# Performance work log

Measured on AMD Instinct MI355X. Metric: run time of the kernel, lower is better.

The kernel has to match this reference:

```python
import jax, jax.numpy as jnp
import numpy as np

N_NODES = 100000
N_EDGES = 800000
IN_CH = 128
HID = 128
OUT_CH = 64


def setup_inputs() -> dict:
    key = jax.random.key(0)
    ks = jax.random.split(key, 8)
    x = jax.random.normal(ks[0], (N_NODES, IN_CH), dtype=jnp.float32)
    edge_index = jax.random.randint(ks[1], (2, N_EDGES), 0, N_NODES, dtype=jnp.int64)
    # GCNConv weights (Glorot) and zero biases
    def glorot(k, fan_in, fan_out):
        s = jnp.sqrt(6.0 / (fan_in + fan_out))
        return jax.random.uniform(k, (fan_in, fan_out), jnp.float32, -s, s)
    return {
        "x": x,
        "edge_index": edge_index,
        "W1": glorot(ks[2], IN_CH, HID), "b1": jnp.zeros((HID,), jnp.float32),
        "W2": glorot(ks[3], HID, HID),   "b2": jnp.zeros((HID,), jnp.float32),
        "W3": glorot(ks[4], HID, OUT_CH), "b3": jnp.zeros((OUT_CH,), jnp.float32),
    }


def _gcn_conv(h, W, b, src, dst, norm, self_norm, n_nodes):
    """PyG GCNConv: out = D^-1/2 (A+I) D^-1/2 (h W) + b.
    Self-loop contribution added densely (self_norm = dinv^2) to avoid
    appending N extra edges."""
    h = h @ W  # [N, F_out]
    msg = h[src] * norm[:, None]  # [E, F_out] gathered + normalized messages
    agg = jax.ops.segment_sum(msg, dst, num_segments=n_nodes)
    return agg + h * self_norm[:, None] + b


def reference(x, edge_index, W1, b1, W2, b2, W3, b3):
    n_nodes = x.shape[0]
    src = edge_index[0]
    dst = edge_index[1]
    # degrees with self-loops (edge weights = 1)
    deg = jax.ops.segment_sum(jnp.ones_like(src, dtype=x.dtype), dst,
                              num_segments=n_nodes) + 1.0
    dinv = jax.lax.rsqrt(deg)
    norm = dinv[src] * dinv[dst]   # per-edge symmetric normalization
    self_norm = dinv * dinv        # normalization of the i->i self loop

    h = jax.nn.relu(_gcn_conv(x, W1, b1, src, dst, norm, self_norm, n_nodes))
    # dropout is identity in eval mode (training=False)
    h = jax.nn.relu(_gcn_conv(h, W2, b2, src, dst, norm, self_norm, n_nodes))
    out = _gcn_conv(h, W3, b3, src, dst, norm, self_norm, n_nodes)
    return out
```

## Files before the change

kernel.cpp:

```cpp
#include <hip/hip_runtime.h>


#define IN_CH 128

typedef __attribute__((ext_vector_type(8))) short bf16x8;
typedef __attribute__((ext_vector_type(4))) float f32x4;

__device__ inline unsigned short f2bf_rne(float f) {
    unsigned u = __float_as_uint(f);
    unsigned r = (u + 0x7FFFu + ((u >> 16) & 1u)) >> 16;
    return (unsigned short)r;
}
__device__ inline float bf2f(unsigned short h) {
    return __uint_as_float(((unsigned)h) << 16);
}
__device__ inline float bf2f_lo(unsigned m) {
    return __uint_as_float(m << 16);
}
__device__ inline float bf2f_hi(unsigned m) {
    return __uint_as_float(m & 0xffff0000u);
}

__global__ __launch_bounds__(256) void cnt_k(const int* __restrict__ dst,
                                             int* __restrict__ cnt, int E) {
    int e = blockIdx.x * 256 + threadIdx.x;
    if (e < E) atomicAdd(&cnt[dst[e]], 1);
}

__global__ __launch_bounds__(256) void scan1_k(const int* __restrict__ cnt,
                                               int* __restrict__ bsum,
                                               float* __restrict__ dinv, int N) {
    __shared__ int s[256];
    int tid = threadIdx.x;
    int i = blockIdx.x * 256 + tid;
    int v = (i < N) ? cnt[i] : 0;
    if (i < N) dinv[i] = rsqrtf((float)v + 1.0f);
    s[tid] = v;
    __syncthreads();
    for (int off = 128; off > 0; off >>= 1) {
        if (tid < off) s[tid] += s[tid + off];
        __syncthreads();
    }
    if (tid == 0) bsum[blockIdx.x] = s[0];
}

__global__ __launch_bounds__(512) void scan2_k(int* __restrict__ bsum, int nb) {
    __shared__ int s[512];
    __shared__ int carry_s;
    int tid = threadIdx.x;
    if (tid == 0) carry_s = 0;
    __syncthreads();
    for (int base = 0; base < nb; base += 512) {
        int c = carry_s;
        int i = base + tid;
        int v = (i < nb) ? bsum[i] : 0;
        s[tid] = v;
        __syncthreads();
        for (int off = 1; off < 512; off <<= 1) {
            int t = (tid >= off) ? s[tid - off] : 0;
            __syncthreads();
            s[tid] += t;
            __syncthreads();
        }
        if (i < nb) bsum[i] = s[tid] - v + c;
        __syncthreads();
        if (tid == 0) carry_s = c + s[511];
        __syncthreads();
    }
}

__global__ __launch_bounds__(256) void scan3_k(const int* __restrict__ cnt,
                                               const int* __restrict__ bsum,
                                               int* __restrict__ rowptr, int N) {
    __shared__ int s[256];
    int tid = threadIdx.x;
    int i = blockIdx.x * 256 + tid;
    int v = (i < N) ? cnt[i] : 0;
    s[tid] = v;
    __syncthreads();
    for (int off = 1; off < 256; off <<= 1) {
        int t = (tid >= off) ? s[tid - off] : 0;
        __syncthreads();
        s[tid] += t;
        __syncthreads();
    }
    if (i < N) rowptr[i] = s[tid] - v + bsum[blockIdx.x];
}

__device__ inline void convw_one(const float* W, unsigned short* hi, int FOUT, int id) {
    int n = id >> 7, k = id & 127;
    hi[id] = f2bf_rne(W[k * FOUT + n]);
}

__global__ __launch_bounds__(256) void fill_conv_k(
    const int* __restrict__ src, const int* __restrict__ dst,
    const float* __restrict__ dinv, int* __restrict__ rowptr,
    int2* __restrict__ pairs, int E, int fillBlocks,
    const float* __restrict__ W1, const float* __restrict__ W2,
    const float* __restrict__ W3,
    unsigned short* __restrict__ W1h, unsigned short* __restrict__ W2h,
    unsigned short* __restrict__ W3h) {
    if ((int)blockIdx.x < fillBlocks) {
        int e = blockIdx.x * 256 + threadIdx.x;
        if (e < E) {
            int s = src[e], d = dst[e];
            float nrm = dinv[s] * dinv[d];
            int pos = atomicAdd(&rowptr[d], 1);
            pairs[pos] = make_int2(s, __float_as_int(nrm));
        }
    } else {
        int id = (blockIdx.x - fillBlocks) * 256 + threadIdx.x;
        if (id < 16384) convw_one(W1, W1h, 128, id);
        else if (id < 32768) convw_one(W2, W2h, 128, id - 16384);
        else if (id < 40960) convw_one(W3, W3h, 64, id - 32768);
    }
}

__device__ inline bf16x8 cvt8(const float* __restrict__ p) {
    float4 v0 = *(const float4*)p;
    float4 v1 = *(const float4*)(p + 4);
    bf16x8 h;
    h[0] = (short)f2bf_rne(v0.x); h[1] = (short)f2bf_rne(v0.y);
    h[2] = (short)f2bf_rne(v0.z); h[3] = (short)f2bf_rne(v0.w);
    h[4] = (short)f2bf_rne(v1.x); h[5] = (short)f2bf_rne(v1.y);
    h[6] = (short)f2bf_rne(v1.z); h[7] = (short)f2bf_rne(v1.w);
    return h;
}

template <int FOUT, bool AF32>
__global__ __launch_bounds__(256) void mfma_gemm(const float* __restrict__ Af,
                                                 const unsigned short* __restrict__ Ahi,
                                                 const unsigned short* __restrict__ Bhi,
                                                 unsigned short* __restrict__ Thi,
                                                 int N) {
    constexpr int NCT = FOUT / 16;
    constexpr int BSTRIDE = 136;
    constexpr int CSTRIDE = FOUT + 8;
    constexpr int BU = FOUT * BSTRIDE;
    constexpr int CU = 64 * CSTRIDE;
    constexpr int SMEMU = (BU > CU) ? BU : CU;
    __shared__ unsigned short smem[SMEMU];

    const int tid = threadIdx.x;
    const int wv = tid >> 6, lane = tid & 63;
    const int quad = lane >> 4, l16 = lane & 15;
    const int row0 = blockIdx.x * 64 + wv * 16;

#pragma unroll
    for (int it = 0; it < FOUT / 16; ++it) {
        int i = it * 256 + tid;
        int r = i >> 4, c = (i & 15) * 8;
        *(bf16x8*)(&smem[r * BSTRIDE + c]) = *(const bf16x8*)(Bhi + (size_t)r * 128 + c);
    }
    __syncthreads();

    f32x4 acc[NCT];
#pragma unroll
    for (int ct = 0; ct < NCT; ++ct)
        acc[ct] = (f32x4){0.f, 0.f, 0.f, 0.f};

    const int ra = AF32 ? min(row0 + l16, N - 1) : (row0 + l16);

#pragma unroll
    for (int ks = 0; ks < 4; ++ks) {
        const int ko = ks * 32 + quad * 8;
        bf16x8 ah;
        if (AF32) {
            ah = cvt8(Af + (size_t)ra * 128 + ko);
        } else {
            ah = *(const bf16x8*)(Ahi + (size_t)ra * 128 + ko);
        }
#pragma unroll
        for (int ct = 0; ct < NCT; ++ct) {
            bf16x8 bh = *(const bf16x8*)(&smem[(ct * 16 + l16) * BSTRIDE + ko]);
            acc[ct] = __builtin_amdgcn_mfma_f32_16x16x32_bf16(ah, bh, acc[ct], 0, 0, 0);
        }
    }

    __syncthreads();
    const int lrow = wv * 16 + quad * 4;
#pragma unroll
    for (int ct = 0; ct < NCT; ++ct) {
        const int col = ct * 16 + l16;
#pragma unroll
        for (int r = 0; r < 4; ++r)
            smem[(lrow + r) * CSTRIDE + col] = f2bf_rne(acc[ct][r]);
    }
    __syncthreads();
    constexpr int CH = FOUT / 8;
#pragma unroll
    for (int i = 0; i < 64 * CH / 256; ++i) {
        int ci = i * 256 + tid;
        int r = ci / CH, c = (ci % CH) * 8;
        int grow = blockIdx.x * 64 + r;
        if (grow < N)
            *(uint4*)(Thi + (size_t)grow * FOUT + c) = *(const uint4*)&smem[r * CSTRIDE + c];
    }
}

template <int FOUT, bool SPLIT>
__global__ __launch_bounds__(256) void gather_k(const int* __restrict__ rowend,
                                                const int2* __restrict__ pairs,
                                                const float* __restrict__ dinv,
                                                const unsigned short* __restrict__ Thi,
                                                const float* __restrict__ bias,
                                                float* __restrict__ out,
                                                unsigned short* __restrict__ outHi,
                                                int N) {
    const int wave = threadIdx.x >> 6;
    const int lane = threadIdx.x & 63;
    const int row = blockIdx.x * 4 + wave;
    if (row >= N) return;

    const int start = (row == 0) ? 0 : rowend[row - 1];
    const int end = rowend[row];
    const float dr = dinv[row];

    if (FOUT == 128) {
        const unsigned* thi32 = (const unsigned*)Thi;
        unsigned sh = thi32[(size_t)row * 64 + lane];
        float2 bb = *(const float2*)(bias + lane * 2);
        float ax = bb.x + bf2f_lo(sh) * dr * dr;
        float ay = bb.y + bf2f_hi(sh) * dr * dr;

        int j = start;
        if ((j & 1) && j < end) {
            int2 pv = pairs[j];
            unsigned m = thi32[(size_t)pv.x * 64 + lane];
            float n = __int_as_float(pv.y);
            ax += n * bf2f_lo(m);
            ay += n * bf2f_hi(m);
            ++j;
        }
        for (; j + 4 <= end; j += 4) {
            int4 p01 = *(const int4*)(pairs + j);
            int4 p23 = *(const int4*)(pairs + j + 2);
            unsigned m0 = thi32[(size_t)p01.x * 64 + lane];
            unsigned m1 = thi32[(size_t)p01.z * 64 + lane];
            unsigned m2 = thi32[(size_t)p23.x * 64 + lane];
            unsigned m3 = thi32[(size_t)p23.z * 64 + lane];
            float n0 = __int_as_float(p01.y), n1 = __int_as_float(p01.w);
            float n2 = __int_as_float(p23.y), n3 = __int_as_float(p23.w);
            ax += n0 * bf2f_lo(m0); ay += n0 * bf2f_hi(m0);
            ax += n1 * bf2f_lo(m1); ay += n1 * bf2f_hi(m1);
            ax += n2 * bf2f_lo(m2); ay += n2 * bf2f_hi(m2);
            ax += n3 * bf2f_lo(m3); ay += n3 * bf2f_hi(m3);
        }
        for (; j < end; ++j) {
            int2 pv = pairs[j];
            unsigned m = thi32[(size_t)pv.x * 64 + lane];
            float n = __int_as_float(pv.y);
            ax += n * bf2f_lo(m);
            ay += n * bf2f_hi(m);
        }

        if (SPLIT) {
            float vx = fmaxf(ax, 0.f), vy = fmaxf(ay, 0.f);
            ushort2 h;
            h.x = f2bf_rne(vx);
            h.y = f2bf_rne(vy);
            *(ushort2*)(outHi + (size_t)row * 128 + lane * 2) = h;
        } else {
            float2 o; o.x = ax; o.y = ay;
            *(float2*)(out + (size_t)row * 128 + lane * 2) = o;
        }
    } else {
        float acc = bias[lane] + bf2f(Thi[(size_t)row * FOUT + lane]) * dr * dr;

        int j = start;
        if ((j & 1) && j < end) {
            int2 pv = pairs[j];
            acc += __int_as_float(pv.y) * bf2f(Thi[(size_t)pv.x * FOUT + lane]);
            ++j;
        }
        for (; j + 4 <= end; j += 4) {
            int4 p01 = *(const int4*)(pairs + j);
            int4 p23 = *(const int4*)(pairs + j + 2);
            float m0 = bf2f(Thi[(size_t)p01.x * FOUT + lane]);
            float m1 = bf2f(Thi[(size_t)p01.z * FOUT + lane]);
            float m2 = bf2f(Thi[(size_t)p23.x * FOUT + lane]);
            float m3 = bf2f(Thi[(size_t)p23.z * FOUT + lane]);
            acc += __int_as_float(p01.y) * m0 + __int_as_float(p01.w) * m1 +
                   __int_as_float(p23.y) * m2 + __int_as_float(p23.w) * m3;
        }
        for (; j < end; ++j) {
            int2 pv = pairs[j];
            acc += __int_as_float(pv.y) * bf2f(Thi[(size_t)pv.x * FOUT + lane]);
        }
        out[(size_t)row * FOUT + lane] = acc;
    }
}

extern "C" void kernel_launch(void* const* d_in, const int* in_sizes, int n_in,
                              void* d_out, int out_size, void* d_ws, size_t ws_size,
                              hipStream_t stream) {
    const float* x  = (const float*)d_in[0];
    const int* eidx = (const int*)d_in[1];
    const float* W1 = (const float*)d_in[2];
    const float* b1 = (const float*)d_in[3];
    const float* W2 = (const float*)d_in[4];
    const float* b2 = (const float*)d_in[5];
    const float* W3 = (const float*)d_in[6];
    const float* b3 = (const float*)d_in[7];
    float* out = (float*)d_out;

    const int N = in_sizes[0] / IN_CH;
    const int E = in_sizes[1] / 2;
    const int* src = eidx;
    const int* dst = eidx + E;
    const int Npad = ((N + 127) / 128) * 128;
    const int nb = (N + 255) / 256;

    auto align = [](size_t v) { return (v + 255) / 256 * 256; };
    char* p = (char*)d_ws;
    int* cnt = (int*)p;            p += align((size_t)N * 4);
    int* rowptr = (int*)p;         p += align((size_t)N * 4);
    int* bsum = (int*)p;           p += align((size_t)nb * 4);
    float* dinv = (float*)p;       p += align((size_t)N * 4);
    int2* pairs = (int2*)p;        p += align((size_t)E * 8);
    unsigned short* Ahi = (unsigned short*)p;  p += align((size_t)Npad * 128 * 2);
    unsigned short* Thi = (unsigned short*)p;  p += align((size_t)Npad * 128 * 2);
    unsigned short* W1h = (unsigned short*)p;  p += align(128 * 128 * 2);
    unsigned short* W2h = (unsigned short*)p;  p += align(128 * 128 * 2);
    unsigned short* W3h = (unsigned short*)p;

    hipMemsetAsync(cnt, 0, (size_t)N * 4, stream);
    cnt_k<<<(E + 255) / 256, 256, 0, stream>>>(dst, cnt, E);
    scan1_k<<<nb, 256, 0, stream>>>(cnt, bsum, dinv, N);
    scan2_k<<<1, 512, 0, stream>>>(bsum, nb);
    scan3_k<<<nb, 256, 0, stream>>>(cnt, bsum, rowptr, N);
    const int fillBlocks = (E + 255) / 256;
    fill_conv_k<<<fillBlocks + 160, 256, 0, stream>>>(src, dst, dinv, rowptr, pairs,
                                                      E, fillBlocks, W1, W2, W3,
                                                      W1h, W2h, W3h);

    const int gemm_blocks = (N + 63) / 64;
    const int gather_blocks = (N + 3) / 4;

    mfma_gemm<128, true><<<gemm_blocks, 256, 0, stream>>>(x, nullptr, W1h, Thi, N);
    gather_k<128, true><<<gather_blocks, 256, 0, stream>>>(rowptr, pairs, dinv, Thi,
                                                           b1, nullptr, Ahi, N);
    mfma_gemm<128, false><<<gemm_blocks, 256, 0, stream>>>(nullptr, Ahi, W2h, Thi, N);
    gather_k<128, true><<<gather_blocks, 256, 0, stream>>>(rowptr, pairs, dinv, Thi,
                                                           b2, nullptr, Ahi, N);
    mfma_gemm<64, false><<<gemm_blocks, 256, 0, stream>>>(nullptr, Ahi, W3h, Thi, N);
    gather_k<64, false><<<gather_blocks, 256, 0, stream>>>(rowptr, pairs, dinv, Thi,
                                                           b3, out, nullptr, N);
}
```

Baseline: 358.9 us.

## Pad CSR rows to multiples of four and prescale source indices to byte offsets

The CSR edge list now pads each destination row to a multiple of four entries. The padding is zero-filled, so it acts as zero-weight edges that gather row 0. The gather kernels drop their alignment-peel and tail loops and run only the unrolled 4-wide loop. Source indices are stored pre-multiplied by the row byte stride, which removes the 64-bit index multiply in the address computation. The cost is a memset of the larger pairs buffer, up to 3N extra padded edges, and a separate cursor array for the atomic fill.

```diff
diff --git a/kernel.cpp b/kernel.cpp
--- a/kernel.cpp
+++ b/kernel.cpp
@@ -33,9 +33,9 @@
     __shared__ int s[256];
     int tid = threadIdx.x;
     int i = blockIdx.x * 256 + tid;
-    int v = (i < N) ? cnt[i] : 0;
-    if (i < N) dinv[i] = rsqrtf((float)v + 1.0f);
-    s[tid] = v;
+    int vr = (i < N) ? cnt[i] : 0;
+    if (i < N) dinv[i] = rsqrtf((float)vr + 1.0f);
+    s[tid] = (i < N) ? ((vr + 3) & ~3) : 0;
     __syncthreads();
     for (int off = 128; off > 0; off >>= 1) {
         if (tid < off) s[tid] += s[tid + off];
@@ -71,11 +71,12 @@
 
 __global__ __launch_bounds__(256) void scan3_k(const int* __restrict__ cnt,
                                                const int* __restrict__ bsum,
-                                               int* __restrict__ rowptr, int N) {
+                                               int* __restrict__ rowstart,
+                                               int* __restrict__ cur, int N) {
     __shared__ int s[256];
     int tid = threadIdx.x;
     int i = blockIdx.x * 256 + tid;
-    int v = (i < N) ? cnt[i] : 0;
+    int v = (i < N) ? ((cnt[i] + 3) & ~3) : 0;
     s[tid] = v;
     __syncthreads();
     for (int off = 1; off < 256; off <<= 1) {
@@ -84,7 +85,12 @@
         s[tid] += t;
         __syncthreads();
     }
-    if (i < N) rowptr[i] = s[tid] - v + bsum[blockIdx.x];
+    if (i < N) {
+        int st = s[tid] - v + bsum[blockIdx.x];
+        rowstart[i] = st;
+        cur[i] = st;
+        if (i == N - 1) rowstart[N] = st + v;
+    }
 }
 
 __device__ inline void convw_one(const float* W, unsigned short* hi, int FOUT, int id) {
@@ -94,7 +100,7 @@
 
 __global__ __launch_bounds__(256) void fill_conv_k(
     const int* __restrict__ src, const int* __restrict__ dst,
-    const float* __restrict__ dinv, int* __restrict__ rowptr,
+    const float* __restrict__ dinv, int* __restrict__ cur,
     int2* __restrict__ pairs, int E, int fillBlocks,
     const float* __restrict__ W1, const float* __restrict__ W2,
     const float* __restrict__ W3,
@@ -105,8 +111,8 @@
         if (e < E) {
             int s = src[e], d = dst[e];
             float nrm = dinv[s] * dinv[d];
-            int pos = atomicAdd(&rowptr[d], 1);
-            pairs[pos] = make_int2(s, __float_as_int(nrm));
+            int pos = atomicAdd(&cur[d], 1);
+            pairs[pos] = make_int2(s * 256, __float_as_int(nrm));
         }
     } else {
         int id = (blockIdx.x - fillBlocks) * 256 + threadIdx.x;
@@ -199,7 +205,7 @@
 }
 
 template <int FOUT, bool SPLIT>
-__global__ __launch_bounds__(256) void gather_k(const int* __restrict__ rowend,
+__global__ __launch_bounds__(256) void gather_k(const int* __restrict__ rowstart,
                                                 const int2* __restrict__ pairs,
                                                 const float* __restrict__ dinv,
                                                 const unsigned short* __restrict__ Thi,
@@ -212,46 +218,31 @@
     const int row = blockIdx.x * 4 + wave;
     if (row >= N) return;
 
-    const int start = (row == 0) ? 0 : rowend[row - 1];
-    const int end = rowend[row];
+    const int start = rowstart[row];
+    const int end = rowstart[row + 1];
     const float dr = dinv[row];
+    const char* tbase = (const char*)Thi;
 
     if (FOUT == 128) {
-        const unsigned* thi32 = (const unsigned*)Thi;
-        unsigned sh = thi32[(size_t)row * 64 + lane];
+        const int laneB = lane * 4;
+        unsigned sh = *(const unsigned*)(tbase + (size_t)row * 256 + laneB);
         float2 bb = *(const float2*)(bias + lane * 2);
         float ax = bb.x + bf2f_lo(sh) * dr * dr;
         float ay = bb.y + bf2f_hi(sh) * dr * dr;
 
-        int j = start;
-        if ((j & 1) && j < end) {
-            int2 pv = pairs[j];
-            unsigned m = thi32[(size_t)pv.x * 64 + lane];
-            float n = __int_as_float(pv.y);
-            ax += n * bf2f_lo(m);
-            ay += n * bf2f_hi(m);
-            ++j;
-        }
-        for (; j + 4 <= end; j += 4) {
+        for (int j = start; j < end; j += 4) {
             int4 p01 = *(const int4*)(pairs + j);
             int4 p23 = *(const int4*)(pairs + j + 2);
-            unsigned m0 = thi32[(size_t)p01.x * 64 + lane];
-            unsigned m1 = thi32[(size_t)p01.z * 64 + lane];
-            unsigned m2 = thi32[(size_t)p23.x * 64 + lane];
-            unsigned m3 = thi32[(size_t)p23.z * 64 + lane];
+            unsigned m0 = *(const unsigned*)(tbase + (unsigned)p01.x + laneB);
+            unsigned m1 = *(const unsigned*)(tbase + (unsigned)p01.z + laneB);
+            unsigned m2 = *(const unsigned*)(tbase + (unsigned)p23.x + laneB);
+            unsigned m3 = *(const unsigned*)(tbase + (unsigned)p23.z + laneB);
             float n0 = __int_as_float(p01.y), n1 = __int_as_float(p01.w);
             float n2 = __int_as_float(p23.y), n3 = __int_as_float(p23.w);
             ax += n0 * bf2f_lo(m0); ay += n0 * bf2f_hi(m0);
             ax += n1 * bf2f_lo(m1); ay += n1 * bf2f_hi(m1);
             ax += n2 * bf2f_lo(m2); ay += n2 * bf2f_hi(m2);
             ax += n3 * bf2f_lo(m3); ay += n3 * bf2f_hi(m3);
-        }
-        for (; j < end; ++j) {
-            int2 pv = pairs[j];
-            unsigned m = thi32[(size_t)pv.x * 64 + lane];
-            float n = __int_as_float(pv.y);
-            ax += n * bf2f_lo(m);
-            ay += n * bf2f_hi(m);
         }
 
         if (SPLIT) {
@@ -265,27 +256,19 @@
             *(float2*)(out + (size_t)row * 128 + lane * 2) = o;
         }
     } else {
-        float acc = bias[lane] + bf2f(Thi[(size_t)row * FOUT + lane]) * dr * dr;
-
-        int j = start;
-        if ((j & 1) && j < end) {
-            int2 pv = pairs[j];
-            acc += __int_as_float(pv.y) * bf2f(Thi[(size_t)pv.x * FOUT + lane]);
-            ++j;
-        }
-        for (; j + 4 <= end; j += 4) {
+        const int laneB = lane * 2;
+        float acc = bias[lane] +
+                    bf2f(*(const unsigned short*)(tbase + (size_t)row * 128 + laneB)) * dr * dr;
+
+        for (int j = start; j < end; j += 4) {
             int4 p01 = *(const int4*)(pairs + j);
             int4 p23 = *(const int4*)(pairs + j + 2);
-            float m0 = bf2f(Thi[(size_t)p01.x * FOUT + lane]);
-            float m1 = bf2f(Thi[(size_t)p01.z * FOUT + lane]);
-            float m2 = bf2f(Thi[(size_t)p23.x * FOUT + lane]);
-            float m3 = bf2f(Thi[(size_t)p23.z * FOUT + lane]);
+            float m0 = bf2f(*(const unsigned short*)(tbase + ((unsigned)p01.x >> 1) + laneB));
+            float m1 = bf2f(*(const unsigned short*)(tbase + ((unsigned)p01.z >> 1) + laneB));
+            float m2 = bf2f(*(const unsigned short*)(tbase + ((unsigned)p23.x >> 1) + laneB));
+            float m3 = bf2f(*(const unsigned short*)(tbase + ((unsigned)p23.z >> 1) + laneB));
             acc += __int_as_float(p01.y) * m0 + __int_as_float(p01.w) * m1 +
                    __int_as_float(p23.y) * m2 + __int_as_float(p23.w) * m3;
-        }
-        for (; j < end; ++j) {
-            int2 pv = pairs[j];
-            acc += __int_as_float(pv.y) * bf2f(Thi[(size_t)pv.x * FOUT + lane]);
         }
         out[(size_t)row * FOUT + lane] = acc;
     }
@@ -310,14 +293,16 @@
     const int* dst = eidx + E;
     const int Npad = ((N + 127) / 128) * 128;
     const int nb = (N + 255) / 256;
+    const int Emax = E + 3 * N;
 
     auto align = [](size_t v) { return (v + 255) / 256 * 256; };
     char* p = (char*)d_ws;
     int* cnt = (int*)p;            p += align((size_t)N * 4);
-    int* rowptr = (int*)p;         p += align((size_t)N * 4);
+    int* rowstart = (int*)p;       p += align((size_t)(N + 1) * 4);
+    int* cur = (int*)p;            p += align((size_t)N * 4);
     int* bsum = (int*)p;           p += align((size_t)nb * 4);
     float* dinv = (float*)p;       p += align((size_t)N * 4);
-    int2* pairs = (int2*)p;        p += align((size_t)E * 8);
+    int2* pairs = (int2*)p;        p += align((size_t)Emax * 8);
     unsigned short* Ahi = (unsigned short*)p;  p += align((size_t)Npad * 128 * 2);
     unsigned short* Thi = (unsigned short*)p;  p += align((size_t)Npad * 128 * 2);
     unsigned short* W1h = (unsigned short*)p;  p += align(128 * 128 * 2);
@@ -325,12 +310,13 @@
     unsigned short* W3h = (unsigned short*)p;
 
     hipMemsetAsync(cnt, 0, (size_t)N * 4, stream);
+    hipMemsetAsync(pairs, 0, (size_t)Emax * 8, stream);
     cnt_k<<<(E + 255) / 256, 256, 0, stream>>>(dst, cnt, E);
     scan1_k<<<nb, 256, 0, stream>>>(cnt, bsum, dinv, N);
     scan2_k<<<1, 512, 0, stream>>>(bsum, nb);
-    scan3_k<<<nb, 256, 0, stream>>>(cnt, bsum, rowptr, N);
+    scan3_k<<<nb, 256, 0, stream>>>(cnt, bsum, rowstart, cur, N);
     const int fillBlocks = (E + 255) / 256;
-    fill_conv_k<<<fillBlocks + 160, 256, 0, stream>>>(src, dst, dinv, rowptr, pairs,
+    fill_conv_k<<<fillBlocks + 160, 256, 0, stream>>>(src, dst, dinv, cur, pairs,
                                                       E, fillBlocks, W1, W2, W3,
                                                       W1h, W2h, W3h);
 
@@ -338,12 +324,12 @@
     const int gather_blocks = (N + 3) / 4;
 
     mfma_gemm<128, true><<<gemm_blocks, 256, 0, stream>>>(x, nullptr, W1h, Thi, N);
-    gather_k<128, true><<<gather_blocks, 256, 0, stream>>>(rowptr, pairs, dinv, Thi,
+    gather_k<128, true><<<gather_blocks, 256, 0, stream>>>(rowstart, pairs, dinv, Thi,
                                                            b1, nullptr, Ahi, N);
     mfma_gemm<128, false><<<gemm_blocks, 256, 0, stream>>>(nullptr, Ahi, W2h, Thi, N);
-    gather_k<128, true><<<gather_blocks, 256, 0, stream>>>(rowptr, pairs, dinv, Thi,
+    gather_k<128, true><<<gather_blocks, 256, 0, stream>>>(rowstart, pairs, dinv, Thi,
                                                            b2, nullptr, Ahi, N);
     mfma_gemm<64, false><<<gemm_blocks, 256, 0, stream>>>(nullptr, Ahi, W3h, Thi, N);
-    gather_k<64, false><<<gather_blocks, 256, 0, stream>>>(rowptr, pairs, dinv, Thi,
+    gather_k<64, false><<<gather_blocks, 256, 0, stream>>>(rowstart, pairs, dinv, Thi,
                                                            b3, out, nullptr, N);
 }
```

Result: faster. 342.4 us (-4.6%).
